# Kernel tuning notes

Measured on AMD Instinct MI355X. Metric: run time of the kernel, lower is better.

## Reference

```python
import jax, jax.numpy as jnp
import numpy as np

N = 8192
F_IN = 256
F_OUT = 64
ALPHA = 0.2  # leaky relu negative slope
MASK_VAL = -9e15


def setup_inputs() -> dict:
    key = jax.random.key(0)
    k1, k2, k3, k4, k5, k6 = jax.random.split(key, 6)
    stdv_lin = 1.0 / np.sqrt(F_IN)
    stdv_a = 1.0 / np.sqrt(2 * F_OUT)
    return {
        "input": jax.random.normal(k1, (N, F_IN), dtype=jnp.float32),
        "adj": jax.random.randint(k2, (N, N), 0, 2, dtype=jnp.int32),
        "W": jax.random.uniform(k3, (F_IN, F_OUT), minval=-stdv_lin, maxval=stdv_lin, dtype=jnp.float32),
        "b_lin": jax.random.uniform(k4, (F_OUT,), minval=-stdv_lin, maxval=stdv_lin, dtype=jnp.float32),
        "a": jax.random.uniform(k5, (2 * F_OUT, 1), minval=-stdv_a, maxval=stdv_a, dtype=jnp.float32),
        "bias": jax.random.uniform(k6, (F_OUT,), minval=-stdv_a, maxval=stdv_a, dtype=jnp.float32),
    }


def reference(input, adj, W, b_lin, a, bias):
    # h = Linear(input): [N, F_OUT]
    h = input @ W + b_lin
    # e[i,j] = leaky_relu(a1 . h_i + a2 . h_j)  (equivalent to the repeat/cat/matmul in torch,
    # without materializing the [N, N, 2*F_OUT] tensor)
    a1 = a[:F_OUT, 0]
    a2 = a[F_OUT:, 0]
    s1 = h @ a1  # [N]
    s2 = h @ a2  # [N]
    e = jax.nn.leaky_relu(s1[:, None] + s2[None, :], negative_slope=ALPHA)  # [N, N]
    attention = jnp.where(adj > 0, e, MASK_VAL)
    attention = jax.nn.softmax(attention, axis=1)
    # dropout is identity in eval mode (training=False)
    output = attention @ h + bias
    return output
```

## Files before the change

kernel.cpp:

```cpp
#include <hip/hip_runtime.h>

#define N 8192
#define FIN 256
#define FOUT 64
#define ALPHA 0.2f
#define LOG2C 4
#define NCHUNK (1 << LOG2C)
#define CLEN (N >> LOG2C)

typedef float f32x4 __attribute__((ext_vector_type(4)));
typedef short s16x8 __attribute__((ext_vector_type(8)));

static __device__ __forceinline__ unsigned short f2bf(float x) {
    unsigned u = __float_as_uint(x);
    u += 0x7fffu + ((u >> 16) & 1u);
    return (unsigned short)(u >> 16);
}

__global__ __launch_bounds__(256) void k_linear(
    const float* __restrict__ input, const float* __restrict__ W,
    const float* __restrict__ b_lin, const float* __restrict__ a,
    unsigned short* __restrict__ hTf, float* __restrict__ s1, float* __restrict__ s2,
    unsigned* __restrict__ s2max_enc)
{
    __shared__ float in_sh[16 * FIN];
    __shared__ float hst[64][17];
    int t = threadIdx.x, w = t >> 6, f = t & 63;
    int b = blockIdx.x;
    int i0 = b * 16;

#pragma unroll
    for (int r = 0; r < 4; r++) {
        int row = w * 4 + r;
        *(float4*)&in_sh[row * FIN + f * 4] =
            *(const float4*)(input + (size_t)(i0 + row) * FIN + f * 4);
    }

    float a1v = a[f], a2v = a[FOUT + f];
    float h[4];
#pragma unroll
    for (int r = 0; r < 4; r++) h[r] = b_lin[f];

    for (int k4 = 0; k4 < FIN / 4; k4++) {
        float wv0 = W[(k4 * 4 + 0) * FOUT + f];
        float wv1 = W[(k4 * 4 + 1) * FOUT + f];
        float wv2 = W[(k4 * 4 + 2) * FOUT + f];
        float wv3 = W[(k4 * 4 + 3) * FOUT + f];
#pragma unroll
        for (int r = 0; r < 4; r++) {
            float4 iv = *(const float4*)&in_sh[(w * 4 + r) * FIN + k4 * 4];
            h[r] = fmaf(iv.x, wv0, h[r]);
            h[r] = fmaf(iv.y, wv1, h[r]);
            h[r] = fmaf(iv.z, wv2, h[r]);
            h[r] = fmaf(iv.w, wv3, h[r]);
        }
    }

    float wmax = -1e30f;
#pragma unroll
    for (int r = 0; r < 4; r++) {
        hst[f][w * 4 + r] = h[r];
        float v1 = h[r] * a1v, v2 = h[r] * a2v;
#pragma unroll
        for (int d = 1; d < 64; d <<= 1) { v1 += __shfl_xor(v1, d); v2 += __shfl_xor(v2, d); }
        wmax = fmaxf(wmax, v2);
        if (f == 0) { s1[i0 + w * 4 + r] = v1; s2[i0 + w * 4 + r] = v2; }
    }
    if (f == 0) {
        unsigned u = __float_as_uint(wmax);
        unsigned key = (u & 0x80000000u) ? ~u : (u | 0x80000000u);
        atomicMax(s2max_enc, key);
    }
    __syncthreads();

    int fo = t >> 2, seg = t & 3;
    unsigned lo = f2bf(hst[fo][seg * 4 + 0]) | ((unsigned)f2bf(hst[fo][seg * 4 + 1]) << 16);
    unsigned hi = f2bf(hst[fo][seg * 4 + 2]) | ((unsigned)f2bf(hst[fo][seg * 4 + 3]) << 16);
    int2 v; v.x = (int)lo; v.y = (int)hi;
    size_t base = (size_t)(b >> 1) * 2048 + (size_t)fo * 32 + (b & 1) * 16 + seg * 4;
    *(int2*)(hTf + base) = v;
}


#define PGEN(AV0, AV1, SVP, AFR) do {                                             \
    float4 sv0 = *(const float4*)(SVP);                                           \
    float4 sv1 = *(const float4*)((SVP) + 4);                                     \
    float p0, p1, p2, p3, p4, p5, p6, p7;                                         \
    { float u = s1c + sv0.x; float g = fmaxf(u, fmaf(0.2f, u, c2)); p0 = (AV0.x > 0) ? exp2f(g) : 0.f; } \
    { float u = s1c + sv0.y; float g = fmaxf(u, fmaf(0.2f, u, c2)); p1 = (AV0.y > 0) ? exp2f(g) : 0.f; } \
    { float u = s1c + sv0.z; float g = fmaxf(u, fmaf(0.2f, u, c2)); p2 = (AV0.z > 0) ? exp2f(g) : 0.f; } \
    { float u = s1c + sv0.w; float g = fmaxf(u, fmaf(0.2f, u, c2)); p3 = (AV0.w > 0) ? exp2f(g) : 0.f; } \
    { float u = s1c + sv1.x; float g = fmaxf(u, fmaf(0.2f, u, c2)); p4 = (AV1.x > 0) ? exp2f(g) : 0.f; } \
    { float u = s1c + sv1.y; float g = fmaxf(u, fmaf(0.2f, u, c2)); p5 = (AV1.y > 0) ? exp2f(g) : 0.f; } \
    { float u = s1c + sv1.z; float g = fmaxf(u, fmaf(0.2f, u, c2)); p6 = (AV1.z > 0) ? exp2f(g) : 0.f; } \
    { float u = s1c + sv1.w; float g = fmaxf(u, fmaf(0.2f, u, c2)); p7 = (AV1.w > 0) ? exp2f(g) : 0.f; } \
    dacc += ((p0 + p1) + (p2 + p3)) + ((p4 + p5) + (p6 + p7));                    \
    union { s16x8 v; unsigned u[4]; } pk;                                         \
    asm("v_cvt_pk_bf16_f32 %0, %1, %2" : "=v"(pk.u[0]) : "v"(p0), "v"(p1));       \
    asm("v_cvt_pk_bf16_f32 %0, %1, %2" : "=v"(pk.u[1]) : "v"(p2), "v"(p3));       \
    asm("v_cvt_pk_bf16_f32 %0, %1, %2" : "=v"(pk.u[2]) : "v"(p4), "v"(p5));       \
    asm("v_cvt_pk_bf16_f32 %0, %1, %2" : "=v"(pk.u[3]) : "v"(p6), "v"(p7));       \
    AFR = pk.v;                                                                   \
} while (0)

#define BODY(AREG, IT) do {                                                       \
    s16x8 afr0, afr1;                                                             \
    const float* svp = &s2sh[(IT) * 64 + kg * 8];                                 \
    PGEN(AREG[0], AREG[1], svp, afr0);                                            \
    PGEN(AREG[2], AREG[3], svp + 32, afr1);                                       \
    if ((IT) + 2 < CLEN / 64) {                                                   \
        AREG[0] = adjq[((IT) + 2) * 16 + kg * 2 + 0];                             \
        AREG[1] = adjq[((IT) + 2) * 16 + kg * 2 + 1];                             \
        AREG[2] = adjq[((IT) + 2) * 16 + 8 + kg * 2 + 0];                         \
        AREG[3] = adjq[((IT) + 2) * 16 + 8 + kg * 2 + 1];                         \
    }                                                                             \
    const unsigned short* bt = hsh + (size_t)((IT) * 2) * 2048 + l15 * 32 + kgs * 8; \
    _Pragma("unroll")                                                             \
    for (int nt = 0; nt < 4; nt++) {                                              \
        const unsigned short* bq = bt + nt * 512;                                 \
        s16x8 b0 = *(const s16x8*)(bq);                                           \
        s16x8 b1 = *(const s16x8*)(bq + 2048);                                    \
        acc[nt] = __builtin_amdgcn_mfma_f32_16x16x32_bf16(afr0, b0, acc[nt], 0, 0, 0); \
        acc[nt] = __builtin_amdgcn_mfma_f32_16x16x32_bf16(afr1, b1, acc[nt], 0, 0, 0); \
    }                                                                             \
} while (0)

__global__ __launch_bounds__(512, 4) void k_attn(
    const int* __restrict__ adj, const float* __restrict__ s1g,
    const float* __restrict__ s2g, const unsigned short* __restrict__ hTf,
    const unsigned* __restrict__ s2max_enc,
    float* __restrict__ numP, float* __restrict__ denP)
{
    extern __shared__ char smem[];
    unsigned short* hsh = (unsigned short*)smem;
    float* s2sh = (float*)(smem + 64 * CLEN * 2);

    const float LOG2E = 1.4426950408889634f;
    int bid = blockIdx.x;
    int chunk = bid & (NCHUNK - 1);
    int rg = bid >> LOG2C;
    int jstart = chunk * CLEN;
    int t = threadIdx.x, w = t >> 6, l = t & 63;
    int l15 = l & 15, kg = l >> 4;
    int kgs = kg ^ ((l15 >> 1) & 3);

    {
        const int4* src = (const int4*)(hTf + (size_t)jstart * 64);
        int4* dst = (int4*)hsh;
#pragma unroll
        for (int k = 0; k < 8; k++) {
            int G = t + k * 512;
            int Gs = (G & ~3) | ((G ^ (G >> 3)) & 3);
            dst[Gs] = src[G];
        }
        s2sh[t] = s2g[jstart + t] * LOG2E;
    }
    unsigned key = *s2max_enc;
    unsigned su = (key & 0x80000000u) ? (key ^ 0x80000000u) : ~key;
    float s2m = __uint_as_float(su);
    __syncthreads();

    int i0 = rg * 128;
    int i = i0 + w * 16 + l15;
    float s1v = s1g[i];
    float mx = s1v + s2m; mx = fmaxf(mx, ALPHA * mx);
    float m2 = mx * LOG2E;
    float s1c = fmaf(s1v, LOG2E, -m2);
    float c2 = -0.8f * m2;

    const int4* adjq = (const int4*)(adj + (size_t)i * N + jstart);
    int4 a0[4], a1[4];
    a0[0] = adjq[kg * 2 + 0];  a0[1] = adjq[kg * 2 + 1];
    a0[2] = adjq[8 + kg * 2 + 0];  a0[3] = adjq[8 + kg * 2 + 1];
    a1[0] = adjq[16 + kg * 2 + 0]; a1[1] = adjq[16 + kg * 2 + 1];
    a1[2] = adjq[24 + kg * 2 + 0]; a1[3] = adjq[24 + kg * 2 + 1];

    f32x4 acc[4] = {};
    float dacc = 0.f;

#pragma unroll 1
    for (int it = 0; it < CLEN / 64; it += 2) {
        BODY(a0, it);
        BODY(a1, it + 1);
    }

    dacc += __shfl_xor(dacc, 16);
    dacc += __shfl_xor(dacc, 32);
    if (l < 16) denP[(size_t)chunk * N + i0 + w * 16 + l] = dacc;
#pragma unroll
    for (int nt = 0; nt < 4; nt++) {
#pragma unroll
        for (int r = 0; r < 4; r++) {
            int orow = w * 16 + kg * 4 + r;
            numP[((size_t)chunk * N + i0 + orow) * FOUT + nt * 16 + l15] = acc[nt][r];
        }
    }
}

__global__ __launch_bounds__(256) void k_finalize(
    const float* __restrict__ numP, const float* __restrict__ denP,
    const float* __restrict__ bias, float* __restrict__ out)
{
    int idx = blockIdx.x * 256 + threadIdx.x;
    int i = idx >> 6, f = idx & 63;
    float nsum = 0.f, dsum = 0.f;
#pragma unroll
    for (int c = 0; c < NCHUNK; c++) {
        nsum += numP[(size_t)c * (N * FOUT) + idx];
        dsum += denP[(size_t)c * N + i];
    }
    out[idx] = nsum / dsum + bias[f];
}

extern "C" void kernel_launch(void* const* d_in, const int* in_sizes, int n_in,
                              void* d_out, int out_size, void* d_ws, size_t ws_size,
                              hipStream_t stream)
{
    const float* input = (const float*)d_in[0];
    const int*   adj   = (const int*)d_in[1];
    const float* W     = (const float*)d_in[2];
    const float* b_lin = (const float*)d_in[3];
    const float* a     = (const float*)d_in[4];
    const float* bias  = (const float*)d_in[5];
    float* out = (float*)d_out;

    char* ws = (char*)d_ws;
    unsigned short* hTf = (unsigned short*)ws;
    float* s1    = (float*)(ws + 1048576);
    float* s2    = (float*)(ws + 1048576 + 32768);
    unsigned* s2max_enc = (unsigned*)(ws + 1048576 + 65536);
    size_t fixed = 1048576 + 65536 + 256;
    float* numP = (float*)(ws + fixed);
    float* denP = (float*)(ws + fixed + ((size_t)N * FOUT * 4) * NCHUNK);

    size_t smem = (size_t)64 * CLEN * 2 + CLEN * 4;
    hipFuncSetAttribute((const void*)k_attn,
                        hipFuncAttributeMaxDynamicSharedMemorySize, (int)smem);

    hipMemsetAsync(s2max_enc, 0, 4, stream);
    hipLaunchKernelGGL(k_linear, dim3(512), dim3(256), 0, stream,
                       input, W, b_lin, a, hTf, s1, s2, s2max_enc);
    hipLaunchKernelGGL(k_attn, dim3((N / 128) * NCHUNK), dim3(512), smem, stream,
                       adj, s1, s2, hTf, s2max_enc, numP, denP);
    hipLaunchKernelGGL(k_finalize, dim3(2048), dim3(256), 0, stream,
                       numP, denP, bias, out);
}
```

Baseline: 109.7 us.

## Stream h tiles through small LDS buffer with smaller blocks and fewer chunks

The attention kernel no longer stages the whole chunk of h in dynamic LDS. Each iteration now loads one 64-column tile of h into a static 8KB buffer, guarded by two barriers per iteration. Blocks shrink to 256 threads covering 64 rows, and the column split drops from 16 to 8 chunks. This cuts LDS use per block to raise occupancy for the adjacency-bandwidth-bound loop. In exchange, h is re-read from cache more often, adjacency prefetch is only one tile deep, and each iteration pays for barriers.

```diff
diff --git a/kernel.cpp b/kernel.cpp
--- a/kernel.cpp
+++ b/kernel.cpp
@@ -4,7 +4,7 @@
 #define FIN 256
 #define FOUT 64
 #define ALPHA 0.2f
-#define LOG2C 4
+#define LOG2C 3
 #define NCHUNK (1 << LOG2C)
 #define CLEN (N >> LOG2C)
 
@@ -103,37 +103,14 @@
     AFR = pk.v;                                                                   \
 } while (0)
 
-#define BODY(AREG, IT) do {                                                       \
-    s16x8 afr0, afr1;                                                             \
-    const float* svp = &s2sh[(IT) * 64 + kg * 8];                                 \
-    PGEN(AREG[0], AREG[1], svp, afr0);                                            \
-    PGEN(AREG[2], AREG[3], svp + 32, afr1);                                       \
-    if ((IT) + 2 < CLEN / 64) {                                                   \
-        AREG[0] = adjq[((IT) + 2) * 16 + kg * 2 + 0];                             \
-        AREG[1] = adjq[((IT) + 2) * 16 + kg * 2 + 1];                             \
-        AREG[2] = adjq[((IT) + 2) * 16 + 8 + kg * 2 + 0];                         \
-        AREG[3] = adjq[((IT) + 2) * 16 + 8 + kg * 2 + 1];                         \
-    }                                                                             \
-    const unsigned short* bt = hsh + (size_t)((IT) * 2) * 2048 + l15 * 32 + kgs * 8; \
-    _Pragma("unroll")                                                             \
-    for (int nt = 0; nt < 4; nt++) {                                              \
-        const unsigned short* bq = bt + nt * 512;                                 \
-        s16x8 b0 = *(const s16x8*)(bq);                                           \
-        s16x8 b1 = *(const s16x8*)(bq + 2048);                                    \
-        acc[nt] = __builtin_amdgcn_mfma_f32_16x16x32_bf16(afr0, b0, acc[nt], 0, 0, 0); \
-        acc[nt] = __builtin_amdgcn_mfma_f32_16x16x32_bf16(afr1, b1, acc[nt], 0, 0, 0); \
-    }                                                                             \
-} while (0)
-
-__global__ __launch_bounds__(512, 4) void k_attn(
+__global__ __launch_bounds__(256) void k_attn(
     const int* __restrict__ adj, const float* __restrict__ s1g,
     const float* __restrict__ s2g, const unsigned short* __restrict__ hTf,
     const unsigned* __restrict__ s2max_enc,
     float* __restrict__ numP, float* __restrict__ denP)
 {
-    extern __shared__ char smem[];
-    unsigned short* hsh = (unsigned short*)smem;
-    float* s2sh = (float*)(smem + 64 * CLEN * 2);
+    __shared__ unsigned short hsh[4096];
+    __shared__ float s2sh[CLEN];
 
     const float LOG2E = 1.4426950408889634f;
     int bid = blockIdx.x;
@@ -145,22 +122,15 @@
     int kgs = kg ^ ((l15 >> 1) & 3);
 
     {
-        const int4* src = (const int4*)(hTf + (size_t)jstart * 64);
-        int4* dst = (int4*)hsh;
-#pragma unroll
-        for (int k = 0; k < 8; k++) {
-            int G = t + k * 512;
-            int Gs = (G & ~3) | ((G ^ (G >> 3)) & 3);
-            dst[Gs] = src[G];
-        }
-        s2sh[t] = s2g[jstart + t] * LOG2E;
+        float4 sv = ((const float4*)(s2g + jstart))[t];
+        sv.x *= LOG2E; sv.y *= LOG2E; sv.z *= LOG2E; sv.w *= LOG2E;
+        ((float4*)s2sh)[t] = sv;
     }
     unsigned key = *s2max_enc;
     unsigned su = (key & 0x80000000u) ? (key ^ 0x80000000u) : ~key;
     float s2m = __uint_as_float(su);
-    __syncthreads();
-
-    int i0 = rg * 128;
+
+    int i0 = rg * 64;
     int i = i0 + w * 16 + l15;
     float s1v = s1g[i];
     float mx = s1v + s2m; mx = fmaxf(mx, ALPHA * mx);
@@ -169,19 +139,63 @@
     float c2 = -0.8f * m2;
 
     const int4* adjq = (const int4*)(adj + (size_t)i * N + jstart);
-    int4 a0[4], a1[4];
-    a0[0] = adjq[kg * 2 + 0];  a0[1] = adjq[kg * 2 + 1];
-    a0[2] = adjq[8 + kg * 2 + 0];  a0[3] = adjq[8 + kg * 2 + 1];
-    a1[0] = adjq[16 + kg * 2 + 0]; a1[1] = adjq[16 + kg * 2 + 1];
-    a1[2] = adjq[24 + kg * 2 + 0]; a1[3] = adjq[24 + kg * 2 + 1];
+    const int4* src4 = (const int4*)(hTf + (size_t)jstart * 64);
+
+    int4 a0 = adjq[kg * 2 + 0];
+    int4 a1 = adjq[kg * 2 + 1];
+    int4 a2 = adjq[8 + kg * 2 + 0];
+    int4 a3 = adjq[8 + kg * 2 + 1];
 
     f32x4 acc[4] = {};
     float dacc = 0.f;
 
 #pragma unroll 1
-    for (int it = 0; it < CLEN / 64; it += 2) {
-        BODY(a0, it);
-        BODY(a1, it + 1);
+    for (int it = 0; it < CLEN / 64; it++) {
+        if (it) __syncthreads();
+        {
+            int G0 = t, G1 = t + 256;
+            int4 v0 = src4[it * 512 + G0];
+            int4 v1 = src4[it * 512 + G1];
+            ((int4*)hsh)[(G0 & ~3) | ((G0 ^ (G0 >> 3)) & 3)] = v0;
+            ((int4*)hsh)[(G1 & ~3) | ((G1 ^ (G1 >> 3)) & 3)] = v1;
+        }
+        __syncthreads();
+
+        int4 n0, n1, n2, n3;
+        if (it + 1 < CLEN / 64) {
+            n0 = adjq[(it + 1) * 16 + kg * 2 + 0];
+            n1 = adjq[(it + 1) * 16 + kg * 2 + 1];
+            n2 = adjq[(it + 1) * 16 + 8 + kg * 2 + 0];
+            n3 = adjq[(it + 1) * 16 + 8 + kg * 2 + 1];
+        }
+
+        const float* svp = &s2sh[it * 64 + kg * 8];
+        const unsigned short* bt = hsh + l15 * 32 + kgs * 8;
+        {
+            s16x8 afr;
+            PGEN(a0, a1, svp, afr);
+            s16x8 b0 = *(const s16x8*)(bt);
+            s16x8 b1 = *(const s16x8*)(bt + 512);
+            s16x8 b2 = *(const s16x8*)(bt + 1024);
+            s16x8 b3 = *(const s16x8*)(bt + 1536);
+            acc[0] = __builtin_amdgcn_mfma_f32_16x16x32_bf16(afr, b0, acc[0], 0, 0, 0);
+            acc[1] = __builtin_amdgcn_mfma_f32_16x16x32_bf16(afr, b1, acc[1], 0, 0, 0);
+            acc[2] = __builtin_amdgcn_mfma_f32_16x16x32_bf16(afr, b2, acc[2], 0, 0, 0);
+            acc[3] = __builtin_amdgcn_mfma_f32_16x16x32_bf16(afr, b3, acc[3], 0, 0, 0);
+        }
+        {
+            s16x8 afr;
+            PGEN(a2, a3, svp + 32, afr);
+            s16x8 b0 = *(const s16x8*)(bt + 2048);
+            s16x8 b1 = *(const s16x8*)(bt + 2560);
+            s16x8 b2 = *(const s16x8*)(bt + 3072);
+            s16x8 b3 = *(const s16x8*)(bt + 3584);
+            acc[0] = __builtin_amdgcn_mfma_f32_16x16x32_bf16(afr, b0, acc[0], 0, 0, 0);
+            acc[1] = __builtin_amdgcn_mfma_f32_16x16x32_bf16(afr, b1, acc[1], 0, 0, 0);
+            acc[2] = __builtin_amdgcn_mfma_f32_16x16x32_bf16(afr, b2, acc[2], 0, 0, 0);
+            acc[3] = __builtin_amdgcn_mfma_f32_16x16x32_bf16(afr, b3, acc[3], 0, 0, 0);
+        }
+        a0 = n0; a1 = n1; a2 = n2; a3 = n3;
     }
 
     dacc += __shfl_xor(dacc, 16);
@@ -233,14 +247,10 @@
     float* numP = (float*)(ws + fixed);
     float* denP = (float*)(ws + fixed + ((size_t)N * FOUT * 4) * NCHUNK);
 
-    size_t smem = (size_t)64 * CLEN * 2 + CLEN * 4;
-    hipFuncSetAttribute((const void*)k_attn,
-                        hipFuncAttributeMaxDynamicSharedMemorySize, (int)smem);
-
     hipMemsetAsync(s2max_enc, 0, 4, stream);
     hipLaunchKernelGGL(k_linear, dim3(512), dim3(256), 0, stream,
                        input, W, b_lin, a, hTf, s1, s2, s2max_enc);
-    hipLaunchKernelGGL(k_attn, dim3((N / 128) * NCHUNK), dim3(512), smem, stream,
+    hipLaunchKernelGGL(k_attn, dim3((N / 64) * NCHUNK), dim3(256), 0, stream,
                        adj, s1, s2, hTf, s2max_enc, numP, denP);
     hipLaunchKernelGGL(k_finalize, dim3(2048), dim3(256), 0, stream,
                        numP, denP, bias, out);
```

After: 103.1 us. 6.0% less time.
